# Kernel optimization log

Hardware: AMD Instinct MI355X
Metric: run time of the kernel (lower is better)

The kernel has to match this reference:

```python
import jax, jax.numpy as jnp
from jax import lax
import numpy as np

POOLING_COUNTS = [15, 8, 8, 8]
N = 128          # segment_num
GROUPS = 4       # GroupNorm groups
TOPK = 5
NMS_THRESH = 0.5
EPS = 1e-5


def _build_structure(pooling_counts, n):
    """Static (numpy) replication of SparseMaxPool's mask2d and pooling schedule."""
    mask2d = np.zeros((n, n), dtype=bool)
    mask2d[np.arange(n), np.arange(n)] = True
    kinds = ['k2'] * pooling_counts[0]
    for c in pooling_counts[1:]:
        kinds += ['k3'] + ['k2'] * (c - 1)
    steps, stride, offset, k = [], 1, 0, 0
    for c in pooling_counts:
        for _ in range(c):
            offset += stride
            i = np.arange(0, n - offset, stride)
            j = np.arange(offset, n, stride)
            mask2d[i, j] = True
            steps.append((kinds[k], i, j))
            k += 1
        stride *= 2
    return mask2d, steps


_MASK2D, _STEPS = _build_structure(POOLING_COUNTS, N)


def sparse_max_pool(x):
    # x: [B, D, N] -> map2d: [B, D, N, N]
    B, D, _ = x.shape
    d = np.arange(N)
    map2d = jnp.zeros((B, D, N, N), x.dtype).at[:, :, d, d].set(x)
    for kind, i, j in _STEPS:
        if kind == 'k2':      # MaxPool1d(kernel=2, stride=1)
            x = jnp.maximum(x[..., :-1], x[..., 1:])
        else:                 # MaxPool1d(kernel=3, stride=2)
            m = jnp.maximum(jnp.maximum(x[..., :-2], x[..., 1:-1]), x[..., 2:])
            x = m[..., ::2]
        map2d = map2d.at[:, :, i, j].set(x)
    return map2d


def group_norm(x, gamma, beta):
    B, C, H, W = x.shape
    xg = x.reshape(B, GROUPS, C // GROUPS, H, W)
    mu = xg.mean(axis=(2, 3, 4), keepdims=True)
    var = xg.var(axis=(2, 3, 4), keepdims=True)
    xn = ((xg - mu) * lax.rsqrt(var + EPS)).reshape(B, C, H, W)
    return xn * gamma[None, :, None, None] + beta[None, :, None, None]


def decode(map2d, conv1_w, gn_gamma, gn_beta, conv2_w, conv2_b):
    dn = ('NCHW', 'OIHW', 'NCHW')
    h = lax.conv_general_dilated(map2d, conv1_w, (1, 1), [(1, 1), (1, 1)], dimension_numbers=dn)
    h = jax.nn.relu(group_norm(h, gn_gamma, gn_beta))
    out = lax.conv_general_dilated(h, conv2_w, (1, 1), [(0, 0), (0, 0)], dimension_numbers=dn)
    return out + conv2_b[None, :, None, None]


def greedy_nms(moments, scores):
    # moments: [M, 2] (start, end); scores: [M]
    M = moments.shape[0]
    order = jnp.argsort(-scores)
    m = moments[order]
    starts, ends = m[:, 0], m[:, 1]
    ar = jnp.arange(M)

    def body(i, sup):
        inter = jnp.clip(jnp.minimum(ends, ends[i]) - jnp.maximum(starts, starts[i]), 0.0)
        union = jnp.maximum(ends, ends[i]) - jnp.minimum(starts, starts[i])
        iou = inter / union
        newly = (iou > NMS_THRESH) & (ar > i) & jnp.logical_not(sup[i])
        return sup | newly

    sup = lax.fori_loop(0, M - 1, body, jnp.zeros((M,), bool))
    keep = jnp.logical_not(sup)
    # first TOPK kept rows in sorted order (static shape)
    pri = jnp.where(keep, M - ar, 0)
    _, idx = lax.top_k(pri, TOPK)
    return m[idx]


def reference(fea, duration, conv1_w, gn_gamma, gn_beta, conv2_w, conv2_b):
    map2d = sparse_max_pool(fea)
    out = decode(map2d, conv1_w, gn_gamma, gn_beta, conv2_w, conv2_b)
    mask = jnp.asarray(_MASK2D, out.dtype)
    score2d = (jax.nn.sigmoid(out) * mask)[0, 0]           # [N, N]
    # score2d_to_moments_scores: nonzero of masked map == static nonzero of mask2d
    gi, gj = np.nonzero(_MASK2D)                            # row-major, matches torch.nonzero
    scores = score2d[gi, gj]                                # [M]
    dur = float(duration)
    moments = jnp.asarray(
        np.stack([gi * (dur / N), (gj + 1) * (dur / N)], axis=-1), jnp.float32
    )                                                       # [M, 2]
    return greedy_nms(moments, scores)                      # [TOPK, 2]


def setup_inputs() -> dict:
    key = jax.random.key(0)
    k0, k1, k2 = jax.random.split(key, 3)
    D = 768
    return {
        'fea': jax.random.normal(k0, (1, D, N), jnp.float32),
        'duration': 30,
        'conv1_w': jax.random.normal(k1, (D, D, 3, 3), jnp.float32) * 0.02,
        'gn_gamma': jnp.ones((D,), jnp.float32),
        'gn_beta': jnp.zeros((D,), jnp.float32),
        'conv2_w': jax.random.normal(k2, (1, D, 1, 1), jnp.float32) * 0.02,
        'conv2_b': jnp.zeros((1,), jnp.float32),
    }
```

## Files before the change

### kernel.cpp

```cpp
#include <hip/hip_runtime.h>
#include <math.h>

#define NPIX 128
#define MASKM 2548
#define NPAD 2560
#define MG   6912
#define KD   768

typedef __attribute__((ext_vector_type(8))) short bf16x8;
typedef __attribute__((ext_vector_type(4))) float f32x4;
typedef __attribute__((ext_vector_type(16))) float f32x16;
typedef __attribute__((ext_vector_type(8))) unsigned short ushort8;

static constexpr size_t OFF_QI   = 0;
static constexpr size_t OFF_QJ   = OFF_QI + NPAD * 4;
static constexpr size_t OFF_QIDX = OFF_QJ + NPAD * 4;
static constexpr size_t OFF_BAR  = OFF_QIDX + 16384 * 4;
static constexpr size_t OFF_LIST = OFF_BAR + 128 * 4;
static constexpr size_t OFF_PART = OFF_LIST + 16384 * 4;
static constexpr size_t OFF_SC   = OFF_PART + 512 * 8 * 8;
static constexpr size_t OFF_HM   = OFF_SC + NPAD * 4;
static constexpr size_t OFF_AH   = OFF_HM + (size_t)MASKM * KD * 4;
static constexpr size_t OFF_AL   = OFF_AH + (size_t)MG * KD * 2;
static constexpr size_t OFF_BH   = OFF_AL + (size_t)MG * KD * 2;
static constexpr size_t OFF_BL   = OFF_BH + (size_t)NPAD * KD * 2;
static constexpr size_t OFF_YT   = OFF_BL + (size_t)NPAD * KD * 2;

__device__ __forceinline__ unsigned short f2bf(float f) {
    unsigned u = __float_as_uint(f);
    u = u + 0x7FFFu + ((u >> 16) & 1u);
    return (unsigned short)(u >> 16);
}
__device__ __forceinline__ float bf2f(unsigned short h) {
    return __uint_as_float(((unsigned)h) << 16);
}

__device__ __forceinline__ bool mask_allowed(int i, int d) {
    if (d == 0) return true;
    if (d <= 15) return true;
    if (d <= 31) return (d >= 17) && ((d & 1) == 1) && ((i & 1) == 0);
    if (d <= 63) return (d >= 35) && ((d & 3) == 3) && ((i & 3) == 0);
    return (d >= 71) && ((d & 7) == 7) && ((i & 7) == 0);
}
__device__ __forceinline__ bool masked_ij(int i, int j) {
    return (j >= i) && (j < NPIX) && (i >= 0) && mask_allowed(i, j - i);
}

__device__ __forceinline__ int row_cnt(int i) {
    int rem = NPIX - i;
    int c1 = rem < 16 ? rem : 16;
    int h2 = (rem - 1) < 31 ? (rem - 1) : 31;
    int c2 = (((i & 1) == 0) && h2 >= 17) ? ((h2 - 17) >> 1) + 1 : 0;
    int h3 = (rem - 1) < 63 ? (rem - 1) : 63;
    int c3 = (((i & 3) == 0) && h3 >= 35) ? ((h3 - 35) >> 2) + 1 : 0;
    int h4 = rem - 1;
    int c4 = (((i & 7) == 0) && h4 >= 71) ? ((h4 - 71) >> 3) + 1 : 0;
    return c1 + c2 + c3 + c4;
}
__device__ __forceinline__ int rank_fwd(int i, int d) {
    int rem = NPIX - i;
    int c1 = rem < 16 ? rem : 16;
    if (d < 16) return d;
    int h2 = (rem - 1) < 31 ? (rem - 1) : 31;
    int c2 = (((i & 1) == 0) && h2 >= 17) ? ((h2 - 17) >> 1) + 1 : 0;
    if (d <= 31) return c1 + ((d - 17) >> 1);
    int h3 = (rem - 1) < 63 ? (rem - 1) : 63;
    int c3 = (((i & 3) == 0) && h3 >= 35) ? ((h3 - 35) >> 2) + 1 : 0;
    if (d <= 63) return c1 + c2 + ((d - 35) >> 2);
    return c1 + c2 + c3 + ((d - 71) >> 3);
}
__device__ __forceinline__ int rank_to_d(int i, int r) {
    int rem = NPIX - i;
    int c1 = rem < 16 ? rem : 16;
    if (r < c1) return r;
    r -= c1;
    int h2 = (rem - 1) < 31 ? (rem - 1) : 31;
    int c2 = (((i & 1) == 0) && h2 >= 17) ? ((h2 - 17) >> 1) + 1 : 0;
    if (r < c2) return 17 + 2 * r;
    r -= c2;
    int h3 = (rem - 1) < 63 ? (rem - 1) : 63;
    int c3 = (((i & 3) == 0) && h3 >= 35) ? ((h3 - 35) >> 2) + 1 : 0;
    if (r < c3) return 35 + 4 * r;
    r -= c3;
    return 71 + 8 * r;
}

#define PREP_LDS 37888
#define PASTR 148

__global__ __launch_bounds__(256) void k_prep(const float* __restrict__ fea,
                                              const float* __restrict__ w1,
                                              int* __restrict__ qi, int* __restrict__ qj,
                                              int* __restrict__ qidx,
                                              double* __restrict__ part, int* __restrict__ bar,
                                              int* __restrict__ list,
                                              unsigned short* __restrict__ Ah,
                                              unsigned short* __restrict__ Al,
                                              unsigned short* __restrict__ Bh,
                                              unsigned short* __restrict__ Bl) {
    extern __shared__ char smp[];
    int tid = threadIdx.x;
    int bid = blockIdx.x;

    if (bid < 64) {
        int* startv = (int*)smp;
        if (tid == 0) {
            int s = 0;
            for (int r = 0; r < NPIX; ++r) { startv[r] = s; s += row_cnt(r); }
        }
        __syncthreads();
        int p = bid * 256 + tid;
        int i = p >> 7, j = p & 127;
        if (masked_ij(i, j)) {
            int q = startv[i] + rank_fwd(i, j - i);
            qi[q] = i; qj[q] = j;
            qidx[p] = q;
        } else {
            qidx[p] = -1;
        }
        int act = 0;
        #pragma unroll
        for (int dy = -1; dy <= 1; ++dy)
            #pragma unroll
            for (int dx = -1; dx <= 1; ++dx)
                if (masked_ij(i + dy, j + dx)) act = 1;
        if (act) { int idx = atomicAdd(&bar[3], 1); list[idx] = p; }
        if (bid == 0 && tid < 8) part[tid] = 0.0;
    } else if (bid < 160) {
        float* tab = (float*)smp;
        int* startv = (int*)(smp + 32768);
        int cb = bid - 64, c0 = cb * 8;
        if (tid == 0) {
            int s = 0;
            for (int r = 0; r < NPIX; ++r) { startv[r] = s; s += row_cnt(r); }
            startv[NPIX] = s;
        }
        for (int idx = tid; idx < 8 * NPIX; idx += 256) {
            int c = idx >> 7, x = idx & 127;
            tab[(c * 8) * 128 + x] = fea[(size_t)(c0 + c) * NPIX + x];
        }
        __syncthreads();
        for (int lvl = 1; lvl < 8; ++lvl) {
            int half = 1 << (lvl - 1), full = 1 << lvl;
            for (int idx = tid; idx < 8 * NPIX; idx += 256) {
                int c = idx >> 7, x = idx & 127;
                if (x + full <= NPIX)
                    tab[(c * 8 + lvl) * 128 + x] =
                        fmaxf(tab[(c * 8 + lvl - 1) * 128 + x],
                              tab[(c * 8 + lvl - 1) * 128 + x + half]);
            }
            __syncthreads();
        }
        for (int q = tid; q < NPAD; q += 256) {
            ushort8 vh = {}, vl = {};
            if (q < MASKM) {
                int i = 0;
                #pragma unroll
                for (int s = 64; s >= 1; s >>= 1) {
                    int cand = i + s;
                    if (cand <= 127 && startv[cand] <= q) i = cand;
                }
                int d = rank_to_d(i, q - startv[i]);
                int j = i + d;
                int len = d + 1;
                int lvl = 31 - __clz(len);
                int x2 = j + 1 - (1 << lvl);
                #pragma unroll
                for (int c = 0; c < 8; ++c) {
                    float v = fmaxf(tab[(c * 8 + lvl) * 128 + i], tab[(c * 8 + lvl) * 128 + x2]);
                    unsigned short hh = f2bf(v);
                    vh[c] = hh; vl[c] = f2bf(v - bf2f(hh));
                }
            }
            *(ushort8*)(Bh + (size_t)q * KD + c0) = vh;
            *(ushort8*)(Bl + (size_t)q * KD + c0) = vl;
        }
    } else {
        float* tile = (float*)smp;
        int pb = bid - 160;
        int co0 = (pb % 12) * 64, ci0 = ((pb / 12) % 12) * 64;
        int s = pb / 144;
        int cib = ci0 + s * 16;
        for (int idx = tid; idx < 2304; idx += 256) {
            int row = idx / 36, c4 = idx % 36;
            float4 v = *(const float4*)(w1 + (size_t)(co0 + row) * MG + cib * 9 + c4 * 4);
            *(float4*)&tile[row * PASTR + c4 * 4] = v;
        }
        __syncthreads();
        for (int idx = tid; idx < 1152; idx += 256) {
            int tap = idx / 128;
            int rem = idx - tap * 128;
            int co = rem >> 1, half = rem & 1;
            ushort8 vh, vl;
            #pragma unroll
            for (int c = 0; c < 8; ++c) {
                float v = tile[co * PASTR + (half * 8 + c) * 9 + tap];
                unsigned short hi = f2bf(v);
                vh[c] = hi;
                vl[c] = f2bf(v - bf2f(hi));
            }
            size_t ob = (size_t)(tap * 768 + co0 + co) * KD + cib + half * 8;
            *(ushort8*)(Ah + ob) = vh;
            *(ushort8*)(Al + ob) = vl;
        }
    }
}

#define BUFSZ   73728
#define SB_BH   32768

__global__ __launch_bounds__(512, 1) void k_gemm(const unsigned short* __restrict__ Ah,
                                                 const unsigned short* __restrict__ Al,
                                                 const unsigned short* __restrict__ Bh,
                                                 const unsigned short* __restrict__ Bl,
                                                 float* __restrict__ Yt) {
    extern __shared__ char sm[];
    int tid = threadIdx.x;
    int wave = tid >> 6, lane = tid & 63;

    int bid = (int)blockIdx.x;
    int xcd = bid & 7, loc = bid >> 3;
    int m0 = loc * 256, n0 = xcd * 320;

    int wm = (wave & 3) << 6, wn = (wave >> 2) * 160;
    int r32 = lane & 31, hi2 = lane >> 5;
    int rb  = (r32 >> 4) * 1024 + hi2 * 256 + (r32 & 15) * 16;
    int awb = (wm >> 4) * 1024 + rb;
    int bwb = (wn >> 4) * 1024 + rb;

    int lrow = lane & 15, lchk = lane >> 4;
    const unsigned short* sp[9];
    int so[9];
    #pragma unroll
    for (int s = 0; s < 9; ++s) {
        int gid = wave * 9 + s;
        const unsigned short* base;
        int row0, ldso;
        if (gid < 16)      { base = Ah; row0 = m0 + gid * 16;        ldso = gid * 1024; }
        else if (gid < 32) { base = Al; row0 = m0 + (gid - 16) * 16; ldso = 16384 + (gid - 16) * 1024; }
        else if (gid < 52) { base = Bh; row0 = n0 + (gid - 32) * 16; ldso = SB_BH + (gid - 32) * 1024; }
        else               { base = Bl; row0 = n0 + (gid - 52) * 16; ldso = SB_BH + 20480 + (gid - 52) * 1024; }
        sp[s] = base + (size_t)(row0 + lrow) * KD + lchk * 8;
        so[s] = ldso;
    }

    f32x16 acc[2][5] = {};
    char* CB = sm;
    char* NB = sm + BUFSZ;

    #define STAGE(DST, s, koff) __builtin_amdgcn_global_load_lds( \
        (const __attribute__((address_space(1))) unsigned int*)(sp[s] + (koff)), \
        (__attribute__((address_space(3))) unsigned int*)((DST) + so[s]), 16, 0, 0)
    #define ARD(hl, mf, ks) (*(const bf16x8*)(CB + (hl) * 16384 + awb + (mf) * 2048 + (ks) * 512))
    #define BRD(hl, nf, ks) (*(const bf16x8*)(CB + SB_BH + (hl) * 20480 + bwb + (nf) * 2048 + (ks) * 512))
    #define TRIP(mf, nf, xh, xl, yh, yl) \
        acc[mf][nf] = __builtin_amdgcn_mfma_f32_32x32x16_bf16(xh, yh, acc[mf][nf], 0, 0, 0); \
        acc[mf][nf] = __builtin_amdgcn_mfma_f32_32x32x16_bf16(xh, yl, acc[mf][nf], 0, 0, 0); \
        acc[mf][nf] = __builtin_amdgcn_mfma_f32_32x32x16_bf16(xl, yh, acc[mf][nf], 0, 0, 0);
    #define RBAR __builtin_amdgcn_s_barrier()
    #define SB0  __builtin_amdgcn_sched_barrier(0)
    #define CL6(nf, xh0, xl0, xh1, xl1, yh, yl) \
        __builtin_amdgcn_s_setprio(1); \
        TRIP(0, nf, xh0, xl0, yh, yl) \
        TRIP(1, nf, xh1, xl1, yh, yl) \
        __builtin_amdgcn_s_setprio(0);

    #pragma unroll
    for (int s = 0; s < 9; ++s) STAGE(CB, s, 0);
    __syncthreads();

    for (int t = 0; t < 24; ++t) {
        int kn = (t + 1) * 32;
        bool stg = (t < 23);
        bf16x8 a0h, a0l, a1h, a1l;
        bf16x8 c0h, c0l, c1h, c1l;
        bf16x8 bxh, bxl, byh, byl;

        a0h = ARD(0, 0, 0); a0l = ARD(1, 0, 0);
        a1h = ARD(0, 1, 0); a1l = ARD(1, 1, 0);
        bxh = BRD(0, 0, 0); bxl = BRD(1, 0, 0);
        if (stg) { STAGE(NB, 0, kn); STAGE(NB, 1, kn); STAGE(NB, 2, kn); }
        RBAR;

        byh = BRD(0, 1, 0); byl = BRD(1, 1, 0);
        SB0;
        CL6(0, a0h, a0l, a1h, a1l, bxh, bxl)
        RBAR;
        bxh = BRD(0, 2, 0); bxl = BRD(1, 2, 0);
        SB0;
        CL6(1, a0h, a0l, a1h, a1l, byh, byl)
        RBAR;
        byh = BRD(0, 3, 0); byl = BRD(1, 3, 0);
        if (stg) { STAGE(NB, 3, kn); STAGE(NB, 4, kn); }
        SB0;
        CL6(2, a0h, a0l, a1h, a1l, bxh, bxl)
        RBAR;
        bxh = BRD(0, 4, 0); bxl = BRD(1, 4, 0);
        SB0;
        CL6(3, a0h, a0l, a1h, a1l, byh, byl)
        RBAR;
        c0h = ARD(0, 0, 1); c0l = ARD(1, 0, 1);
        c1h = ARD(0, 1, 1); c1l = ARD(1, 1, 1);
        byh = BRD(0, 0, 1); byl = BRD(1, 0, 1);
        if (stg) { STAGE(NB, 5, kn); STAGE(NB, 6, kn); }
        SB0;
        CL6(4, a0h, a0l, a1h, a1l, bxh, bxl)
        RBAR;
        bxh = BRD(0, 1, 1); bxl = BRD(1, 1, 1);
        SB0;
        CL6(0, c0h, c0l, c1h, c1l, byh, byl)
        RBAR;
        byh = BRD(0, 2, 1); byl = BRD(1, 2, 1);
        if (stg) { STAGE(NB, 7, kn); STAGE(NB, 8, kn); }
        SB0;
        CL6(1, c0h, c0l, c1h, c1l, bxh, bxl)
        RBAR;
        bxh = BRD(0, 3, 1); bxl = BRD(1, 3, 1);
        SB0;
        CL6(2, c0h, c0l, c1h, c1l, byh, byl)
        RBAR;
        byh = BRD(0, 4, 1); byl = BRD(1, 4, 1);
        SB0;
        CL6(3, c0h, c0l, c1h, c1l, bxh, bxl)
        RBAR;
        CL6(4, c0h, c0l, c1h, c1l, byh, byl)

        __syncthreads();
        char* tmp = CB; CB = NB; NB = tmp;
    }

    #pragma unroll
    for (int mf = 0; mf < 2; ++mf)
        #pragma unroll
        for (int nf = 0; nf < 5; ++nf) {
            int n = n0 + wn + nf * 32 + r32;
            size_t rowb = (size_t)n * MG + m0 + wm + mf * 32 + 4 * hi2;
            #pragma unroll
            for (int g = 0; g < 4; ++g) {
                f32x4 v = { acc[mf][nf][g * 4 + 0], acc[mf][nf][g * 4 + 1],
                            acc[mf][nf][g * 4 + 2], acc[mf][nf][g * 4 + 3] };
                *(f32x4*)(Yt + rowb + 8 * g) = v;
            }
        }
    #undef STAGE
    #undef ARD
    #undef BRD
    #undef TRIP
    #undef RBAR
    #undef SB0
    #undef CL6
}

#define GSN_LDS 44544

__global__ __launch_bounds__(256, 3) void k_gsn(const float* __restrict__ Yt,
                                                const int* __restrict__ qidx,
                                                const int* __restrict__ list,
                                                const float* __restrict__ gamma,
                                                const float* __restrict__ beta,
                                                const float* __restrict__ w2,
                                                const float* __restrict__ b2,
                                                const int* __restrict__ qi,
                                                const int* __restrict__ qj,
                                                const int* __restrict__ durp,
                                                double* __restrict__ part,
                                                int* __restrict__ bar,
                                                float* __restrict__ hm,
                                                float* __restrict__ scores,
                                                float* __restrict__ out) {
    extern __shared__ char smf[];
    int tid = threadIdx.x;
    int bid = (int)blockIdx.x;
    int wave = tid >> 6, lane = tid & 63;

    {
        double* red1 = (double*)smf;
        double* red2 = red1 + 1024;
        double a1[3] = {0, 0, 0}, a2[3] = {0, 0, 0};
        int gs[3];
        #pragma unroll
        for (int s = 0; s < 3; ++s) gs[s] = (64 * s + lane) / 48;

        int nact = bar[3];
        for (int wid = bid * 4 + wave; wid < nact; wid += 637 * 4) {
            int p = list[wid];
            int y = p >> 7, x = p & 127;
            float4 hv[3] = {};
            #pragma unroll
            for (int tap = 0; tap < 9; ++tap) {
                int i = y + tap / 3 - 1, j = x + tap % 3 - 1;
                if ((unsigned)i < 128u && (unsigned)j < 128u) {
                    int q = qidx[i * NPIX + j];
                    if (q >= 0) {
                        const float* yr = Yt + (size_t)q * MG + tap * 768 + lane * 4;
                        #pragma unroll
                        for (int s = 0; s < 3; ++s) {
                            float4 v = *(const float4*)(yr + s * 256);
                            hv[s].x += v.x; hv[s].y += v.y; hv[s].z += v.z; hv[s].w += v.w;
                        }
                    }
                }
            }
            int qp = qidx[p];
            if (qp >= 0) {
                #pragma unroll
                for (int s = 0; s < 3; ++s)
                    *(float4*)(hm + (size_t)qp * KD + s * 256 + lane * 4) = hv[s];
            }
            #pragma unroll
            for (int s = 0; s < 3; ++s) {
                a1[s] += (double)hv[s].x + (double)hv[s].y + (double)hv[s].z + (double)hv[s].w;
                a2[s] += (double)hv[s].x * hv[s].x + (double)hv[s].y * hv[s].y +
                         (double)hv[s].z * hv[s].z + (double)hv[s].w * hv[s].w;
            }
        }
        #pragma unroll
        for (int g = 0; g < 4; ++g) { red1[tid * 4 + g] = 0.0; red2[tid * 4 + g] = 0.0; }
        #pragma unroll
        for (int s = 0; s < 3; ++s) { red1[tid * 4 + gs[s]] = a1[s]; red2[tid * 4 + gs[s]] = a2[s]; }
        __syncthreads();
        if (tid < 8) {
            int g = tid & 3;
            double s = 0.0;
            if (tid < 4) { for (int i = 0; i < 256; ++i) s += red1[i * 4 + g]; }
            else         { for (int i = 0; i < 256; ++i) s += red2[i * 4 + g]; }
            atomicAdd(&part[tid], s);
        }
    }

    __syncthreads();
    if (tid == 0) {
        __hip_atomic_fetch_add(&bar[0], 1, __ATOMIC_RELEASE, __HIP_MEMORY_SCOPE_AGENT);
        while (__hip_atomic_load(&bar[0], __ATOMIC_RELAXED, __HIP_MEMORY_SCOPE_AGENT) < 637)
            __builtin_amdgcn_s_sleep(8);
        (void)__hip_atomic_load(&bar[0], __ATOMIC_ACQUIRE, __HIP_MEMORY_SCOPE_AGENT);
    }
    __syncthreads();

    {
        float mu[4], rs[4];
        const double cnt = 192.0 * 16384.0;
        #pragma unroll
        for (int g = 0; g < 4; ++g) {
            double m = part[g] / cnt;
            double v = part[4 + g] / cnt - m * m;
            mu[g] = (float)m;
            rs[g] = (float)(1.0 / sqrt(v + 1e-5));
        }
        int q = bid * 4 + wave;
        const float* hp = hm + (size_t)q * KD;
        float s = 0.f;
        for (int c = lane; c < KD; c += 64) {
            int g = c / 192;
            float v = (hp[c] - mu[g]) * rs[g] * gamma[c] + beta[c];
            s += fmaxf(v, 0.f) * w2[c];
        }
        for (int o = 32; o; o >>= 1) s += __shfl_down(s, o, 64);
        if (lane == 0) scores[q] = 1.f / (1.f + expf(-(s + b2[0])));
    }
    __syncthreads();
    if (tid == 0)
        __hip_atomic_fetch_add(&bar[1], 1, __ATOMIC_RELEASE, __HIP_MEMORY_SCOPE_AGENT);
    if (bid != 0) return;

    if (tid == 0) {
        while (__hip_atomic_load(&bar[1], __ATOMIC_RELAXED, __HIP_MEMORY_SCOPE_AGENT) < 637)
            __builtin_amdgcn_s_sleep(8);
        (void)__hip_atomic_load(&bar[1], __ATOMIC_ACQUIRE, __HIP_MEMORY_SCOPE_AGENT);
    }
    __syncthreads();

    {
        unsigned long long* key = (unsigned long long*)smf;
        float* ss = (float*)(smf + 20384);
        float* ee = (float*)(smf + 30576);
        unsigned char* st = (unsigned char*)(smf + 40768);
        unsigned long long* wm0 = (unsigned long long*)(smf + 43328);
        unsigned long long* wm1 = (unsigned long long*)(smf + 43360);
        __shared__ int sh_keeper, keepq[5];
        __shared__ float sh_s0, sh_e0;

        float delta = (float)(*durp) / 128.f;
        for (int i = tid; i < MASKM; i += 256) {
            unsigned sb = __float_as_uint(scores[i]);
            key[i] = ((unsigned long long)sb << 32) | (unsigned)(4095 - i);
            ss[i] = qi[i] * delta;
            ee[i] = (qj[i] + 1) * delta;
            st[i] = 0;
        }
        __syncthreads();
        for (int round = 0; round < 5; ++round) {
            unsigned long long b0 = 0, b1 = 0;
            for (int i = tid; i < MASKM; i += 256) {
                unsigned char s = st[i];
                unsigned long long k = key[i];
                if (s == 0) { if (k > b0) b0 = k; }
                else if (s == 1) { if (k > b1) b1 = k; }
            }
            for (int o = 32; o; o >>= 1) {
                unsigned lo0 = __shfl_down((unsigned)b0, o, 64);
                unsigned hi0 = __shfl_down((unsigned)(b0 >> 32), o, 64);
                unsigned long long u0 = ((unsigned long long)hi0 << 32) | lo0;
                unsigned lo1 = __shfl_down((unsigned)b1, o, 64);
                unsigned hi1 = __shfl_down((unsigned)(b1 >> 32), o, 64);
                unsigned long long u1 = ((unsigned long long)hi1 << 32) | lo1;
                if (u0 > b0) b0 = u0;
                if (u1 > b1) b1 = u1;
            }
            if ((tid & 63) == 0) { wm0[tid >> 6] = b0; wm1[tid >> 6] = b1; }
            __syncthreads();
            if (tid == 0) {
                unsigned long long B0 = 0, B1 = 0;
                for (int w = 0; w < 4; ++w) {
                    if (wm0[w] > B0) B0 = wm0[w];
                    if (wm1[w] > B1) B1 = wm1[w];
                }
                int keeper = (B0 != 0);
                unsigned long long B = keeper ? B0 : B1;
                int q = 4095 - (int)(B & 0xFFFFFFFFull);
                st[q] = keeper ? 2 : 3;
                sh_keeper = keeper;
                sh_s0 = ss[q]; sh_e0 = ee[q];
                keepq[round] = q;
            }
            __syncthreads();
            if (sh_keeper) {
                float s0 = sh_s0, e0 = sh_e0;
                for (int i = tid; i < MASKM; i += 256) {
                    if (st[i] == 0) {
                        float inter = fminf(ee[i], e0) - fmaxf(ss[i], s0);
                        if (inter > 0.f) {
                            float uni = fmaxf(ee[i], e0) - fminf(ss[i], s0);
                            if (inter / uni > 0.5f) st[i] = 1;
                        }
                    }
                }
            }
            __syncthreads();
        }
        if (tid < 5) { out[tid * 2] = ss[keepq[tid]]; out[tid * 2 + 1] = ee[keepq[tid]]; }
    }
}

extern "C" void kernel_launch(void* const* d_in, const int* in_sizes, int n_in,
                              void* d_out, int out_size, void* d_ws, size_t ws_size,
                              hipStream_t stream) {
    const float* fea   = (const float*)d_in[0];
    const int*   dur   = (const int*)d_in[1];
    const float* w1    = (const float*)d_in[2];
    const float* gamma = (const float*)d_in[3];
    const float* beta  = (const float*)d_in[4];
    const float* w2    = (const float*)d_in[5];
    const float* b2    = (const float*)d_in[6];
    float* out = (float*)d_out;

    char* ws = (char*)d_ws;
    int*    qi     = (int*)(ws + OFF_QI);
    int*    qj     = (int*)(ws + OFF_QJ);
    int*    qidx   = (int*)(ws + OFF_QIDX);
    int*    bar    = (int*)(ws + OFF_BAR);
    int*    list   = (int*)(ws + OFF_LIST);
    double* part   = (double*)(ws + OFF_PART);
    float*  scores = (float*)(ws + OFF_SC);
    float*  hm     = (float*)(ws + OFF_HM);
    unsigned short* AhU = (unsigned short*)(ws + OFF_AH);
    unsigned short* AlU = (unsigned short*)(ws + OFF_AL);
    unsigned short* BhU = (unsigned short*)(ws + OFF_BH);
    unsigned short* BlU = (unsigned short*)(ws + OFF_BL);
    float*  Yt     = (float*)(ws + OFF_YT);

    static bool attr_set = false;
    if (!attr_set) {
        hipFuncSetAttribute((const void*)k_prep,
                            hipFuncAttributeMaxDynamicSharedMemorySize, PREP_LDS);
        hipFuncSetAttribute((const void*)k_gemm,
                            hipFuncAttributeMaxDynamicSharedMemorySize, 2 * BUFSZ);
        hipFuncSetAttribute((const void*)k_gsn,
                            hipFuncAttributeMaxDynamicSharedMemorySize, GSN_LDS);
        attr_set = true;
    }

    hipMemsetAsync(bar, 0, 16, stream);
    k_prep<<<736, 256, PREP_LDS, stream>>>(fea, w1, qi, qj, qidx, part, bar,
                                           list, AhU, AlU, BhU, BlU);
    k_gemm<<<216, 512, 2 * BUFSZ, stream>>>(AhU, AlU, BhU, BlU, Yt);
    k_gsn<<<637, 256, GSN_LDS, stream>>>(Yt, qidx, list, gamma, beta, w2, b2,
                                         qi, qj, dur, part, bar, hm, scores, out);
}
```

Baseline: 279.7 us.

## Split fused gather/score kernel and replace grid barrier with kernel boundary

Measured after the change: 242.7 us. 1.15x faster.

```diff
diff --git a/kernel.cpp b/kernel.cpp
--- a/kernel.cpp
+++ b/kernel.cpp
@@ -351,91 +351,85 @@
     #undef CL6
 }
 
-#define GSN_LDS 44544
-
-__global__ __launch_bounds__(256, 3) void k_gsn(const float* __restrict__ Yt,
+__global__ __launch_bounds__(256) void k_gather(const float* __restrict__ Yt,
                                                 const int* __restrict__ qidx,
                                                 const int* __restrict__ list,
-                                                const float* __restrict__ gamma,
-                                                const float* __restrict__ beta,
-                                                const float* __restrict__ w2,
-                                                const float* __restrict__ b2,
-                                                const int* __restrict__ qi,
-                                                const int* __restrict__ qj,
-                                                const int* __restrict__ durp,
-                                                double* __restrict__ part,
-                                                int* __restrict__ bar,
+                                                const int* __restrict__ bar,
                                                 float* __restrict__ hm,
-                                                float* __restrict__ scores,
-                                                float* __restrict__ out) {
+                                                double* __restrict__ part) {
+    __shared__ double red1[256 * 4], red2[256 * 4];
+    int tid = threadIdx.x;
+    int wave = tid >> 6, lane = tid & 63;
+    double a1[3] = {0, 0, 0}, a2[3] = {0, 0, 0};
+    int gs[3];
+    #pragma unroll
+    for (int s = 0; s < 3; ++s) gs[s] = (64 * s + lane) / 48;
+
+    int nact = bar[3];
+    for (int wid = blockIdx.x * 4 + wave; wid < nact; wid += gridDim.x * 4) {
+        int p = list[wid];
+        int y = p >> 7, x = p & 127;
+        float4 hv[3] = {};
+        #pragma unroll
+        for (int tap = 0; tap < 9; ++tap) {
+            int i = y + tap / 3 - 1, j = x + tap % 3 - 1;
+            if ((unsigned)i < 128u && (unsigned)j < 128u) {
+                int q = qidx[i * NPIX + j];
+                if (q >= 0) {
+                    const float* yr = Yt + (size_t)q * MG + tap * 768 + lane * 4;
+                    #pragma unroll
+                    for (int s = 0; s < 3; ++s) {
+                        float4 v = *(const float4*)(yr + s * 256);
+                        hv[s].x += v.x; hv[s].y += v.y; hv[s].z += v.z; hv[s].w += v.w;
+                    }
+                }
+            }
+        }
+        int qp = qidx[p];
+        if (qp >= 0) {
+            #pragma unroll
+            for (int s = 0; s < 3; ++s)
+                *(float4*)(hm + (size_t)qp * KD + s * 256 + lane * 4) = hv[s];
+        }
+        #pragma unroll
+        for (int s = 0; s < 3; ++s) {
+            a1[s] += (double)hv[s].x + (double)hv[s].y + (double)hv[s].z + (double)hv[s].w;
+            a2[s] += (double)hv[s].x * hv[s].x + (double)hv[s].y * hv[s].y +
+                     (double)hv[s].z * hv[s].z + (double)hv[s].w * hv[s].w;
+        }
+    }
+    #pragma unroll
+    for (int g = 0; g < 4; ++g) { red1[tid * 4 + g] = 0.0; red2[tid * 4 + g] = 0.0; }
+    #pragma unroll
+    for (int s = 0; s < 3; ++s) { red1[tid * 4 + gs[s]] = a1[s]; red2[tid * 4 + gs[s]] = a2[s]; }
+    __syncthreads();
+    if (tid < 8) {
+        int g = tid & 3;
+        double s = 0.0;
+        if (tid < 4) { for (int i = 0; i < 256; ++i) s += red1[i * 4 + g]; }
+        else         { for (int i = 0; i < 256; ++i) s += red2[i * 4 + g]; }
+        atomicAdd(&part[tid], s);
+    }
+}
+
+#define SNMS_LDS 44544
+
+__global__ __launch_bounds__(256) void k_scorenms(const float* __restrict__ hm,
+                                                  const double* __restrict__ part,
+                                                  const float* __restrict__ gamma,
+                                                  const float* __restrict__ beta,
+                                                  const float* __restrict__ w2,
+                                                  const float* __restrict__ b2,
+                                                  float* __restrict__ scores,
+                                                  const int* __restrict__ qi,
+                                                  const int* __restrict__ qj,
+                                                  const int* __restrict__ durp,
+                                                  int* __restrict__ bar,
+                                                  float* __restrict__ out) {
     extern __shared__ char smf[];
     int tid = threadIdx.x;
     int bid = (int)blockIdx.x;
-    int wave = tid >> 6, lane = tid & 63;
-
-    {
-        double* red1 = (double*)smf;
-        double* red2 = red1 + 1024;
-        double a1[3] = {0, 0, 0}, a2[3] = {0, 0, 0};
-        int gs[3];
-        #pragma unroll
-        for (int s = 0; s < 3; ++s) gs[s] = (64 * s + lane) / 48;
-
-        int nact = bar[3];
-        for (int wid = bid * 4 + wave; wid < nact; wid += 637 * 4) {
-            int p = list[wid];
-            int y = p >> 7, x = p & 127;
-            float4 hv[3] = {};
-            #pragma unroll
-            for (int tap = 0; tap < 9; ++tap) {
-                int i = y + tap / 3 - 1, j = x + tap % 3 - 1;
-                if ((unsigned)i < 128u && (unsigned)j < 128u) {
-                    int q = qidx[i * NPIX + j];
-                    if (q >= 0) {
-                        const float* yr = Yt + (size_t)q * MG + tap * 768 + lane * 4;
-                        #pragma unroll
-                        for (int s = 0; s < 3; ++s) {
-                            float4 v = *(const float4*)(yr + s * 256);
-                            hv[s].x += v.x; hv[s].y += v.y; hv[s].z += v.z; hv[s].w += v.w;
-                        }
-                    }
-                }
-            }
-            int qp = qidx[p];
-            if (qp >= 0) {
-                #pragma unroll
-                for (int s = 0; s < 3; ++s)
-                    *(float4*)(hm + (size_t)qp * KD + s * 256 + lane * 4) = hv[s];
-            }
-            #pragma unroll
-            for (int s = 0; s < 3; ++s) {
-                a1[s] += (double)hv[s].x + (double)hv[s].y + (double)hv[s].z + (double)hv[s].w;
-                a2[s] += (double)hv[s].x * hv[s].x + (double)hv[s].y * hv[s].y +
-                         (double)hv[s].z * hv[s].z + (double)hv[s].w * hv[s].w;
-            }
-        }
-        #pragma unroll
-        for (int g = 0; g < 4; ++g) { red1[tid * 4 + g] = 0.0; red2[tid * 4 + g] = 0.0; }
-        #pragma unroll
-        for (int s = 0; s < 3; ++s) { red1[tid * 4 + gs[s]] = a1[s]; red2[tid * 4 + gs[s]] = a2[s]; }
-        __syncthreads();
-        if (tid < 8) {
-            int g = tid & 3;
-            double s = 0.0;
-            if (tid < 4) { for (int i = 0; i < 256; ++i) s += red1[i * 4 + g]; }
-            else         { for (int i = 0; i < 256; ++i) s += red2[i * 4 + g]; }
-            atomicAdd(&part[tid], s);
-        }
-    }
-
-    __syncthreads();
-    if (tid == 0) {
-        __hip_atomic_fetch_add(&bar[0], 1, __ATOMIC_RELEASE, __HIP_MEMORY_SCOPE_AGENT);
-        while (__hip_atomic_load(&bar[0], __ATOMIC_RELAXED, __HIP_MEMORY_SCOPE_AGENT) < 637)
-            __builtin_amdgcn_s_sleep(8);
-        (void)__hip_atomic_load(&bar[0], __ATOMIC_ACQUIRE, __HIP_MEMORY_SCOPE_AGENT);
-    }
-    __syncthreads();
+    int lane = tid & 63;
 
     {
         float mu[4], rs[4];
@@ -447,7 +441,7 @@
             mu[g] = (float)m;
             rs[g] = (float)(1.0 / sqrt(v + 1e-5));
         }
-        int q = bid * 4 + wave;
+        int q = bid * 4 + (tid >> 6);
         const float* hp = hm + (size_t)q * KD;
         float s = 0.f;
         for (int c = lane; c < KD; c += 64) {
@@ -460,13 +454,13 @@
     }
     __syncthreads();
     if (tid == 0)
-        __hip_atomic_fetch_add(&bar[1], 1, __ATOMIC_RELEASE, __HIP_MEMORY_SCOPE_AGENT);
+        __hip_atomic_fetch_add(&bar[2], 1, __ATOMIC_RELEASE, __HIP_MEMORY_SCOPE_AGENT);
     if (bid != 0) return;
 
     if (tid == 0) {
-        while (__hip_atomic_load(&bar[1], __ATOMIC_RELAXED, __HIP_MEMORY_SCOPE_AGENT) < 637)
+        while (__hip_atomic_load(&bar[2], __ATOMIC_RELAXED, __HIP_MEMORY_SCOPE_AGENT) < 637)
             __builtin_amdgcn_s_sleep(8);
-        (void)__hip_atomic_load(&bar[1], __ATOMIC_ACQUIRE, __HIP_MEMORY_SCOPE_AGENT);
+        (void)__hip_atomic_load(&bar[2], __ATOMIC_ACQUIRE, __HIP_MEMORY_SCOPE_AGENT);
     }
     __syncthreads();
 
@@ -575,8 +569,8 @@
                             hipFuncAttributeMaxDynamicSharedMemorySize, PREP_LDS);
         hipFuncSetAttribute((const void*)k_gemm,
                             hipFuncAttributeMaxDynamicSharedMemorySize, 2 * BUFSZ);
-        hipFuncSetAttribute((const void*)k_gsn,
-                            hipFuncAttributeMaxDynamicSharedMemorySize, GSN_LDS);
+        hipFuncSetAttribute((const void*)k_scorenms,
+                            hipFuncAttributeMaxDynamicSharedMemorySize, SNMS_LDS);
         attr_set = true;
     }
 
@@ -584,6 +578,7 @@
     k_prep<<<736, 256, PREP_LDS, stream>>>(fea, w1, qi, qj, qidx, part, bar,
                                            list, AhU, AlU, BhU, BlU);
     k_gemm<<<216, 512, 2 * BUFSZ, stream>>>(AhU, AlU, BhU, BlU, Yt);
-    k_gsn<<<637, 256, GSN_LDS, stream>>>(Yt, qidx, list, gamma, beta, w2, b2,
-                                         qi, qj, dur, part, bar, hm, scores, out);
-}
+    k_gather<<<1536, 256, 0, stream>>>(Yt, qidx, list, bar, hm, part);
+    k_scorenms<<<637, 256, SNMS_LDS, stream>>>(hm, part, gamma, beta, w2, b2,
+                                               scores, qi, qj, dur, bar, out);
+}
```
